# Optimization experiments

Hardware: AMD Instinct MI355X
Metric: run time of the kernel (lower is better)

The kernel has to match this reference:

```python
import jax, jax.numpy as jnp
import numpy as np

N_NODES = 50000


def gin_conv(x, src, dst, W, b, eps=0.0):
    # GINConv: nn((1+eps)*x_i + sum_{j in N(i)} x_j)
    agg = jax.ops.segment_sum(x[src], dst, num_segments=N_NODES)  # [N, D]
    h = (1.0 + eps) * x + agg
    return h @ W + b


def setup_inputs() -> dict:
    key = jax.random.key(0)
    ks = jax.random.split(key, 8)
    n, e = N_NODES, 800000
    d_in, d_h, d_out = 128, 128, 64
    feature = jax.random.normal(ks[0], (n, d_in), dtype=jnp.float32)
    edge_index = jax.random.randint(ks[1], (2, e), 0, n, dtype=jnp.int64)
    s1 = 1.0 / np.sqrt(d_in)
    sh = 1.0 / np.sqrt(d_h)
    W1 = jax.random.normal(ks[2], (d_in, d_h), dtype=jnp.float32) * s1
    b1 = jnp.zeros((d_h,), dtype=jnp.float32)
    Wh = jax.random.normal(ks[3], (d_h, d_h), dtype=jnp.float32) * sh
    bh = jnp.zeros((d_h,), dtype=jnp.float32)
    Wo = jax.random.normal(ks[4], (d_h, d_out), dtype=jnp.float32) * sh
    bo = jnp.zeros((d_out,), dtype=jnp.float32)
    return {"feature": feature, "edge_index": edge_index, "W1": W1, "b1": b1,
            "Wh": Wh, "bh": bh, "Wo": Wo, "bo": bo}


def reference(feature, edge_index, W1, b1, Wh, bh, Wo, bo):
    src, dst = edge_index[0], edge_index[1]
    x = gin_conv(feature, src, dst, W1, b1)
    x = jax.nn.relu(x)
    # one hidden layer (layer_num=3); dropout disabled (eval)
    x = gin_conv(x, src, dst, Wh, bh)
    x = jax.nn.relu(x)
    x = gin_conv(x, src, dst, Wo, bo)
    return jax.nn.log_softmax(x, axis=1)
```

## Files before the change

### kernel.cpp

```cpp
#include <hip/hip_runtime.h>

typedef short short8 __attribute__((ext_vector_type(8)));
typedef float f32x4 __attribute__((ext_vector_type(4)));


__device__ inline unsigned short f2bf(float f) {
    union { float f; unsigned u; } v; v.f = f;
    unsigned r = v.u + 0x7fffu + ((v.u >> 16) & 1u);
    return (unsigned short)(r >> 16);
}
__device__ inline unsigned pack2(float a, float b) {
    return (unsigned)f2bf(a) | ((unsigned)f2bf(b) << 16);
}
__device__ inline float bflo(unsigned u) { union { unsigned q; float f; } c; c.q = u << 16; return c.f; }
__device__ inline float bfhi(unsigned u) { union { unsigned q; float f; } c; c.q = u & 0xffff0000u; return c.f; }

#define ACC8(vv)                                     \
    acc[0] += bflo(vv.x); acc[1] += bfhi(vv.x);      \
    acc[2] += bflo(vv.y); acc[3] += bfhi(vv.y);      \
    acc[4] += bflo(vv.z); acc[5] += bfhi(vv.z);      \
    acc[6] += bflo(vv.w); acc[7] += bfhi(vv.w);

template <int TPN, typename F>
__device__ __forceinline__ void gather_acc(float acc[8], const uint4* __restrict__ x,
                                           int lane, int beg, int end, F geti) {
    int k = beg;
    for (; k + 8 <= end; k += 8) {
        int idx[8];
#pragma unroll
        for (int j = 0; j < 8; j++) idx[j] = geti(k + j);
        uint4 v[8];
#pragma unroll
        for (int j = 0; j < 8; j++) v[j] = x[(size_t)idx[j] * TPN + lane];
#pragma unroll
        for (int j = 0; j < 8; j++) { ACC8(v[j]) }
    }
    for (; k + 4 <= end; k += 4) {
        int i0 = geti(k), i1 = geti(k + 1), i2 = geti(k + 2), i3 = geti(k + 3);
        uint4 v0 = x[(size_t)i0 * TPN + lane];
        uint4 v1 = x[(size_t)i1 * TPN + lane];
        uint4 v2 = x[(size_t)i2 * TPN + lane];
        uint4 v3 = x[(size_t)i3 * TPN + lane];
        ACC8(v0) ACC8(v1) ACC8(v2) ACC8(v3)
    }
    for (; k < end; ++k) {
        uint4 v0 = x[(size_t)geti(k) * TPN + lane];
        ACC8(v0)
    }
}


#define EPB 2048
#define NE 8
#define BSH 9
#define MAXBKT 128
#define DCAP 10240

__global__ __launch_bounds__(256) void mega1(const int* __restrict__ dst, int* __restrict__ cnt2d,
                                             int e, int nbkt, int nblk,
                                             const float4* __restrict__ feat, uint2* __restrict__ featb,
                                             int cvtb, int nf4,
                                             const float* __restrict__ W1, const float* __restrict__ Wh,
                                             const float* __restrict__ Wo,
                                             unsigned short* __restrict__ W1t, unsigned short* __restrict__ Wht,
                                             unsigned short* __restrict__ Wot) {
    __shared__ int hist[MAXBKT];
    int t = threadIdx.x, b = blockIdx.x;
    if (b < nblk) {
        for (int j = t; j < nbkt; j += 256) hist[j] = 0;
        __syncthreads();
        int base = b * EPB;
#pragma unroll
        for (int j = 0; j < NE; j++) {
            int idx = base + t + 256 * j;
            if (idx < e) atomicAdd(&hist[dst[idx] >> BSH], 1);
        }
        __syncthreads();
        for (int j = t; j < nbkt; j += 256) cnt2d[j * nblk + b] = hist[j];
    } else if (b < nblk + cvtb) {
        int i = (b - nblk) * 256 + t;
        if (i < nf4) {
            float4 v = feat[i];
            featb[i] = make_uint2(pack2(v.x, v.y), pack2(v.z, v.w));
        }
    } else {
        int i = (b - nblk - cvtb) * 256 + t;
        if (i < 16384) {
            int k = i >> 7, nn = i & 127;
            W1t[nn * 128 + k] = f2bf(W1[i]);
        } else if (i < 32768) {
            int j = i - 16384, k = j >> 7, nn = j & 127;
            Wht[nn * 128 + k] = f2bf(Wh[j]);
        } else if (i < 40960) {
            int j = i - 32768, k = j >> 6, nn = j & 63;
            Wot[nn * 128 + k] = f2bf(Wo[j]);
        }
    }
}

__global__ __launch_bounds__(512) void scanB1(int* __restrict__ cnt2d, int* __restrict__ totals, int nblk) {
    __shared__ int s[512];
    int t = threadIdx.x, b = blockIdx.x;
    int v = (t < nblk) ? cnt2d[b * nblk + t] : 0;
    s[t] = v;
    __syncthreads();
    for (int off = 1; off < 512; off <<= 1) {
        int u = (t >= off) ? s[t - off] : 0;
        __syncthreads();
        s[t] += u;
        __syncthreads();
    }
    if (t < nblk) cnt2d[b * nblk + t] = s[t] - v;
    if (t == nblk - 1) totals[b] = s[t];
}

__global__ __launch_bounds__(128) void scanB2(const int* __restrict__ totals, int* __restrict__ bbase,
                                              int* __restrict__ row_ptr, int nbkt, int n, int e) {
    __shared__ int s[128];
    int t = threadIdx.x;
    int v = (t < nbkt) ? totals[t] : 0;
    s[t] = v;
    __syncthreads();
    for (int off = 1; off < 128; off <<= 1) {
        int u = (t >= off) ? s[t - off] : 0;
        __syncthreads();
        s[t] += u;
        __syncthreads();
    }
    if (t < nbkt) bbase[t] = s[t] - v;
    if (t == 0) row_ptr[n] = e;
}

__global__ __launch_bounds__(256) void binC(const int* __restrict__ src, const int* __restrict__ dst,
                                            const int* __restrict__ cnt2d, const int* __restrict__ bbase,
                                            unsigned* __restrict__ pairs, int e, int nbkt, int nblk) {
    __shared__ int hist[MAXBKT], loff[MAXBKT], cur[MAXBKT], gb[MAXBKT];
    __shared__ int sc[256];
    __shared__ unsigned sorted[EPB];
    int t = threadIdx.x, blk = blockIdx.x;
    for (int b = t; b < nbkt; b += 256) hist[b] = 0;
    __syncthreads();
    int base = blk * EPB;
    int cnt = min(EPB, e - base);
    unsigned packed[NE];
    int bb[NE];
#pragma unroll
    for (int j = 0; j < NE; j++) {
        int idx = base + t + 256 * j;
        bb[j] = -1;
        if (idx < e) {
            unsigned s0 = (unsigned)src[idx], d = (unsigned)dst[idx];
            int b = (int)(d >> BSH);
            bb[j] = b;
            packed[j] = s0 | ((d & ((1u << BSH) - 1)) << 16) | ((unsigned)b << 25);
            atomicAdd(&hist[b], 1);
        }
    }
    __syncthreads();
    int v = (t < nbkt) ? hist[t] : 0;
    sc[t] = v;
    __syncthreads();
    for (int off = 1; off < 256; off <<= 1) {
        int u = (t >= off) ? sc[t - off] : 0;
        __syncthreads();
        sc[t] += u;
        __syncthreads();
    }
    if (t < nbkt) {
        int ex = sc[t] - v;
        loff[t] = ex;
        cur[t] = ex;
        gb[t] = bbase[t] + cnt2d[t * nblk + blk];
    }
    __syncthreads();
#pragma unroll
    for (int j = 0; j < NE; j++) {
        if (bb[j] >= 0) {
            int r = atomicAdd(&cur[bb[j]], 1);
            sorted[r] = packed[j];
        }
    }
    __syncthreads();
    for (int i = t; i < cnt; i += 256) {
        unsigned w = sorted[i];
        int b = (int)(w >> 25);
        pairs[gb[b] + (i - loff[b])] = w;
    }
}

__global__ __launch_bounds__(512) void buildD(const unsigned* __restrict__ pairs,
                                              const int* __restrict__ totals, const int* __restrict__ bbase,
                                              int* __restrict__ row_ptr, unsigned short* __restrict__ csr, int n) {
    __shared__ int hist[512], off[512];
    __shared__ unsigned short lcsr[DCAP];
    int t = threadIdx.x, b = blockIdx.x;
    int cnt = totals[b], base = bbase[b];
    hist[t] = 0;
    __syncthreads();
    for (int i = t; i < cnt; i += 512)
        atomicAdd(&hist[(pairs[base + i] >> 16) & 511], 1);
    __syncthreads();
    int v = hist[t];
    off[t] = v;
    __syncthreads();
    for (int o = 1; o < 512; o <<= 1) {
        int u = (t >= o) ? off[t - o] : 0;
        __syncthreads();
        off[t] += u;
        __syncthreads();
    }
    int excl = off[t] - v;
    int node = (b << BSH) + t;
    if (node < n) row_ptr[node] = base + excl;
    __syncthreads();
    hist[t] = excl;
    __syncthreads();
    for (int i = t; i < cnt; i += 512) {
        unsigned w = pairs[base + i];
        int r = atomicAdd(&hist[(w >> 16) & 511], 1);
        if (r < DCAP) lcsr[r] = (unsigned short)(w & 0xFFFFu);
    }
    __syncthreads();
    int lim = min(cnt, DCAP);
    for (int i = t; i < lim; i += 512) csr[base + i] = lcsr[i];
}


#define ECAP 1024

template <bool SECOND>
__global__ __launch_bounds__(256) void fused_layer(
    const uint4* __restrict__ x, const int* __restrict__ row_ptr,
    const unsigned short* __restrict__ csr,
    const short8* __restrict__ Bt, const float* __restrict__ bias,
    unsigned short* __restrict__ out_h,
    const short8* __restrict__ Bt2,
    unsigned short* __restrict__ out_y,
    int n) {
    __shared__ unsigned short As[16][136];
    __shared__ unsigned short Hs[SECOND ? 16 : 1][SECOND ? 136 : 1];
    __shared__ unsigned short eidx[ECAP];

    int t = threadIdx.x;
    int nl = t >> 4, chunk = t & 15;
    int r0 = blockIdx.x * 16;
    int node = r0 + nl;

    int E0 = row_ptr[r0 < n ? r0 : n];
    int E1 = row_ptr[min(r0 + 16, n)];
    int ecnt = min(E1 - E0, ECAP);
    for (int i = t; i < ecnt; i += 256) eidx[i] = csr[E0 + i];
    __syncthreads();

    float acc[8] = {0.f, 0.f, 0.f, 0.f, 0.f, 0.f, 0.f, 0.f};
    if (node < n) {
        uint4 s0 = x[(size_t)node * 16 + chunk];
        ACC8(s0)
        int beg = row_ptr[node], end = row_ptr[node + 1];
        if (end - E0 <= ECAP) {
            gather_acc<16>(acc, x, chunk, beg - E0, end - E0,
                           [&](int k) { return (int)eidx[k]; });
        } else {
            gather_acc<16>(acc, x, chunk, beg, end,
                           [&](int k) { return (int)csr[k]; });
        }
    }
    uint4 packed;
    packed.x = pack2(acc[0], acc[1]); packed.y = pack2(acc[2], acc[3]);
    packed.z = pack2(acc[4], acc[5]); packed.w = pack2(acc[6], acc[7]);
    ((uint4*)&As[nl][0])[chunk] = packed;
    __syncthreads();

    int wid = t >> 6, lane = t & 63;
    int lm = lane & 15, lq = lane >> 4;

    short8 a[4];
#pragma unroll
    for (int kc = 0; kc < 4; kc++)
        a[kc] = *(const short8*)&As[lm][kc * 32 + lq * 8];

    f32x4 hacc[2];
#pragma unroll
    for (int nt = 0; nt < 2; nt++) hacc[nt] = (f32x4){0.f, 0.f, 0.f, 0.f};
#pragma unroll
    for (int nt = 0; nt < 2; nt++) {
        const short8* Br = Bt + (size_t)((wid * 2 + nt) * 16 + lm) * 16;
#pragma unroll
        for (int kc = 0; kc < 4; kc++)
            hacc[nt] = __builtin_amdgcn_mfma_f32_16x16x32_bf16(a[kc], Br[kc * 4 + lq], hacc[nt], 0, 0, 0);
    }

#pragma unroll
    for (int nt = 0; nt < 2; nt++) {
        int col = (wid * 2 + nt) * 16 + lm;
        float bv = bias[col];
#pragma unroll
        for (int i = 0; i < 4; i++) {
            int row = r0 + lq * 4 + i;
            float v = fmaxf(hacc[nt][i] + bv, 0.f);
            if (SECOND) {
                Hs[lq * 4 + i][col] = f2bf(v);
            } else if (row < n) {
                out_h[(size_t)row * 128 + col] = f2bf(v);
            }
        }
    }

    if (SECOND) {
        __syncthreads();
        short8 a2[4];
#pragma unroll
        for (int kc = 0; kc < 4; kc++)
            a2[kc] = *(const short8*)&Hs[lm][kc * 32 + lq * 8];
        f32x4 yacc = (f32x4){0.f, 0.f, 0.f, 0.f};
        const short8* Br2 = Bt2 + (size_t)(wid * 16 + lm) * 16;
#pragma unroll
        for (int kc = 0; kc < 4; kc++)
            yacc = __builtin_amdgcn_mfma_f32_16x16x32_bf16(a2[kc], Br2[kc * 4 + lq], yacc, 0, 0, 0);
        int col = wid * 16 + lm;
#pragma unroll
        for (int i = 0; i < 4; i++) {
            int row = r0 + lq * 4 + i;
            if (row < n) out_y[(size_t)row * 64 + col] = f2bf(yacc[i]);
        }
    }
}


#define ECAP2 1536

__global__ __launch_bounds__(256) void agg_lsm(
    const uint4* __restrict__ x, float* __restrict__ out,
    const int* __restrict__ row_ptr, const unsigned short* __restrict__ csr,
    const float* __restrict__ bo, int n) {
    __shared__ unsigned short eidx[ECAP2];
    int t = threadIdx.x;
    int r0 = blockIdx.x * 32;
    int node = r0 + (t >> 3), lane = t & 7;

    int E0 = row_ptr[r0 < n ? r0 : n];
    int E1 = row_ptr[min(r0 + 32, n)];
    int ecnt = min(E1 - E0, ECAP2);
    for (int i = t; i < ecnt; i += 256) eidx[i] = csr[E0 + i];
    __syncthreads();

    if (node >= n) return;
    uint4 s0 = x[(size_t)node * 8 + lane];
    float acc[8] = { bflo(s0.x), bfhi(s0.x), bflo(s0.y), bfhi(s0.y),
                     bflo(s0.z), bfhi(s0.z), bflo(s0.w), bfhi(s0.w) };
    int beg = row_ptr[node], end = row_ptr[node + 1];
    if (end - E0 <= ECAP2) {
        gather_acc<8>(acc, x, lane, beg - E0, end - E0,
                      [&](int k) { return (int)eidx[k]; });
    } else {
        gather_acc<8>(acc, x, lane, beg, end,
                      [&](int k) { return (int)csr[k]; });
    }

    const float4* bo4 = (const float4*)bo;
    float4 bA = bo4[lane * 2], bB = bo4[lane * 2 + 1];
    acc[0] += bA.x; acc[1] += bA.y; acc[2] += bA.z; acc[3] += bA.w;
    acc[4] += bB.x; acc[5] += bB.y; acc[6] += bB.z; acc[7] += bB.w;
    float m = acc[0];
#pragma unroll
    for (int j = 1; j < 8; j++) m = fmaxf(m, acc[j]);
#pragma unroll
    for (int off = 1; off < 8; off <<= 1) m = fmaxf(m, __shfl_xor(m, off, 64));
    float s = 0.f;
#pragma unroll
    for (int j = 0; j < 8; j++) s += __expf(acc[j] - m);
#pragma unroll
    for (int off = 1; off < 8; off <<= 1) s += __shfl_xor(s, off, 64);
    float ls = m + __logf(s);
    float4 o0 = make_float4(acc[0] - ls, acc[1] - ls, acc[2] - ls, acc[3] - ls);
    float4 o1 = make_float4(acc[4] - ls, acc[5] - ls, acc[6] - ls, acc[7] - ls);
    float4* op = (float4*)(out + (size_t)node * 64 + lane * 8);
    op[0] = o0;
    op[1] = o1;
}


extern "C" void kernel_launch(void* const* d_in, const int* in_sizes, int n_in,
                              void* d_out, int out_size, void* d_ws, size_t ws_size,
                              hipStream_t stream) {
    const float* feature = (const float*)d_in[0];
    const int*   edges   = (const int*)d_in[1];
    const float* W1 = (const float*)d_in[2];
    const float* b1 = (const float*)d_in[3];
    const float* Wh = (const float*)d_in[4];
    const float* bh = (const float*)d_in[5];
    const float* Wo = (const float*)d_in[6];
    const float* bo = (const float*)d_in[7];

    int n = in_sizes[0] / 128;
    int e = in_sizes[1] / 2;
    const int* src = edges;
    const int* dst = edges + e;

    int nbkt = (n + 511) >> BSH;
    int nblk = (e + EPB - 1) / EPB;
    int nf4 = n * 32;
    int cvtb = (nf4 + 255) / 256;

    char* ws = (char*)d_ws;
    auto take = [&](size_t bytes) {
        char* p = ws;
        ws += (bytes + 255) & ~(size_t)255;
        return p;
    };
    int* cnt2d   = (int*)take((size_t)nbkt * nblk * 4);
    int* totals  = (int*)take((size_t)nbkt * 4);
    int* bbase   = (int*)take((size_t)(nbkt + 1) * 4);
    int* row_ptr = (int*)take((size_t)(n + 1) * 4);
    unsigned* pairs = (unsigned*)take((size_t)e * 4);
    unsigned short* csr = (unsigned short*)take((size_t)e * 2);
    unsigned short* featb = (unsigned short*)take((size_t)n * 128 * 2);
    unsigned short* hb    = (unsigned short*)take((size_t)n * 128 * 2);
    unsigned short* yb    = (unsigned short*)take((size_t)n * 64 * 2);
    unsigned short* W1t = (unsigned short*)take(128 * 128 * 2);
    unsigned short* Wht = (unsigned short*)take(128 * 128 * 2);
    unsigned short* Wot = (unsigned short*)take(64 * 128 * 2);

    mega1<<<nblk + cvtb + 160, 256, 0, stream>>>(
        dst, cnt2d, e, nbkt, nblk,
        (const float4*)feature, (uint2*)featb, cvtb, nf4,
        W1, Wh, Wo, W1t, Wht, Wot);
    scanB1<<<nbkt, 512, 0, stream>>>(cnt2d, totals, nblk);
    scanB2<<<1, 128, 0, stream>>>(totals, bbase, row_ptr, nbkt, n, e);
    binC<<<nblk, 256, 0, stream>>>(src, dst, cnt2d, bbase, pairs, e, nbkt, nblk);
    buildD<<<nbkt, 512, 0, stream>>>(pairs, totals, bbase, row_ptr, csr, n);

    int fblocks = (n + 15) / 16;

    fused_layer<false><<<fblocks, 256, 0, stream>>>(
        (const uint4*)featb, row_ptr, csr, (const short8*)W1t, b1,
        hb, nullptr, nullptr, n);

    fused_layer<true><<<fblocks, 256, 0, stream>>>(
        (const uint4*)hb, row_ptr, csr, (const short8*)Wht, bh,
        nullptr, (const short8*)Wot, yb, n);

    agg_lsm<<<(n + 31) / 32, 256, 0, stream>>>(
        (const uint4*)yb, (float*)d_out, row_ptr, csr, bo, n);
}
```

Before: 208.9 us.

## Split fused aggregate+GEMM into column-quarter aggregation and separate MFMA GEMM kernels

Replaces the fused gather+matmul layer kernels with a separate aggregation kernel and a standalone MFMA GEMM. The aggregation kernel splits the feature columns into 64-byte quarters per block, so each block gathers only part of each row, which is meant to improve cache locality and parallelism. The GEMM then reads the aggregated bf16 rows back from global memory. The final layer writes fp32 aggregates for a separate log-softmax kernel. This adds extra global round-trips and kernel launches in exchange for a narrower, more cache-friendly gather.

```diff
diff --git a/kernel.cpp b/kernel.cpp
--- a/kernel.cpp
+++ b/kernel.cpp
@@ -2,6 +2,7 @@
 
 typedef short short8 __attribute__((ext_vector_type(8)));
 typedef float f32x4 __attribute__((ext_vector_type(4)));
+typedef unsigned u32x4 __attribute__((ext_vector_type(4)));
 
 
 __device__ inline unsigned short f2bf(float f) {
@@ -226,141 +227,140 @@
 }
 
 
-#define ECAP 1024
-
-template <bool SECOND>
-__global__ __launch_bounds__(256) void fused_layer(
-    const uint4* __restrict__ x, const int* __restrict__ row_ptr,
-    const unsigned short* __restrict__ csr,
-    const short8* __restrict__ Bt, const float* __restrict__ bias,
-    unsigned short* __restrict__ out_h,
-    const short8* __restrict__ Bt2,
-    unsigned short* __restrict__ out_y,
-    int n) {
-    __shared__ unsigned short As[16][136];
-    __shared__ unsigned short Hs[SECOND ? 16 : 1][SECOND ? 136 : 1];
-    __shared__ unsigned short eidx[ECAP];
-
+#define QECAP 2048
+
+template <int TPN, bool OUTF32>
+__global__ __launch_bounds__(256) void agg_split(
+    const uint4* __restrict__ x, void* __restrict__ outp,
+    const int* __restrict__ row_ptr, const unsigned short* __restrict__ csr,
+    int n, int qblocks) {
+    constexpr int NQ = TPN / 4;
+    __shared__ unsigned short eidx[QECAP];
+    int q = (int)(blockIdx.x % NQ);
+    int nb = (int)(blockIdx.x / NQ);
     int t = threadIdx.x;
-    int nl = t >> 4, chunk = t & 15;
-    int r0 = blockIdx.x * 16;
-    int node = r0 + nl;
-
-    int E0 = row_ptr[r0 < n ? r0 : n];
-    int E1 = row_ptr[min(r0 + 16, n)];
-    int ecnt = min(E1 - E0, ECAP);
-    for (int i = t; i < ecnt; i += 256) eidx[i] = csr[E0 + i];
-    __syncthreads();
+    int r0 = nb * 64;
+
+    int E0 = row_ptr[min(r0, n)], E1 = row_ptr[min(r0 + 64, n)];
+    int ecnt = min(E1 - E0, QECAP);
+    for (int i = t; i < ecnt; i += 256)
+        eidx[i] = __builtin_nontemporal_load(&csr[E0 + i]);
+    __syncthreads();
+
+    int lane = t & 3, slot = t >> 2;
+    int node = r0 + slot;
+    if (node >= n) return;
+    int chunk = q * 4 + lane;
 
     float acc[8] = {0.f, 0.f, 0.f, 0.f, 0.f, 0.f, 0.f, 0.f};
-    if (node < n) {
-        uint4 s0 = x[(size_t)node * 16 + chunk];
-        ACC8(s0)
-        int beg = row_ptr[node], end = row_ptr[node + 1];
-        if (end - E0 <= ECAP) {
-            gather_acc<16>(acc, x, chunk, beg - E0, end - E0,
-                           [&](int k) { return (int)eidx[k]; });
-        } else {
-            gather_acc<16>(acc, x, chunk, beg, end,
-                           [&](int k) { return (int)csr[k]; });
-        }
-    }
-    uint4 packed;
-    packed.x = pack2(acc[0], acc[1]); packed.y = pack2(acc[2], acc[3]);
-    packed.z = pack2(acc[4], acc[5]); packed.w = pack2(acc[6], acc[7]);
-    ((uint4*)&As[nl][0])[chunk] = packed;
-    __syncthreads();
-
-    int wid = t >> 6, lane = t & 63;
-    int lm = lane & 15, lq = lane >> 4;
-
+    uint4 s0 = x[(size_t)node * TPN + chunk];
+    ACC8(s0)
+    int beg = row_ptr[node], end = row_ptr[node + 1];
+    if (E1 - E0 <= QECAP) {
+        gather_acc<TPN>(acc, x, chunk, beg - E0, end - E0,
+                        [&](int k) { return (int)eidx[k]; });
+    } else {
+        gather_acc<TPN>(acc, x, chunk, beg, end,
+                        [&](int k) { return (int)csr[k]; });
+    }
+
+    if (OUTF32) {
+        f32x4* o = (f32x4*)outp + (size_t)node * (TPN * 2) + chunk * 2;
+        f32x4 o0 = {acc[0], acc[1], acc[2], acc[3]};
+        f32x4 o1 = {acc[4], acc[5], acc[6], acc[7]};
+        __builtin_nontemporal_store(o0, o);
+        __builtin_nontemporal_store(o1, o + 1);
+    } else {
+        u32x4 pk = {pack2(acc[0], acc[1]), pack2(acc[2], acc[3]),
+                    pack2(acc[4], acc[5]), pack2(acc[6], acc[7])};
+        __builtin_nontemporal_store(pk, (u32x4*)outp + (size_t)node * TPN + chunk);
+    }
+}
+
+
+template <int OUT, bool SECOND>
+__global__ __launch_bounds__(256) void gemm_mfma(
+    const short8* __restrict__ A, const short8* __restrict__ Bt,
+    const float* __restrict__ bias, unsigned short* __restrict__ outp,
+    const short8* __restrict__ Bt2, unsigned short* __restrict__ out_y, int n) {
+    constexpr int NT = OUT / 16;
+    __shared__ unsigned short Hs[SECOND ? 4 : 1][16][136];
+    int t = threadIdx.x;
+    int wid = t >> 6, lane = t & 63, lm = lane & 15, lq = lane >> 4;
+    int r0 = blockIdx.x * 64 + wid * 16;
+    int arow = min(r0 + lm, n - 1);
+    const short8* Ar = A + (size_t)arow * 16;
     short8 a[4];
 #pragma unroll
-    for (int kc = 0; kc < 4; kc++)
-        a[kc] = *(const short8*)&As[lm][kc * 32 + lq * 8];
-
-    f32x4 hacc[2];
-#pragma unroll
-    for (int nt = 0; nt < 2; nt++) hacc[nt] = (f32x4){0.f, 0.f, 0.f, 0.f};
-#pragma unroll
-    for (int nt = 0; nt < 2; nt++) {
-        const short8* Br = Bt + (size_t)((wid * 2 + nt) * 16 + lm) * 16;
+    for (int kc = 0; kc < 4; kc++) a[kc] = __builtin_nontemporal_load(&Ar[kc * 4 + lq]);
+
+    f32x4 acc[NT];
+#pragma unroll
+    for (int nt = 0; nt < NT; nt++) acc[nt] = (f32x4){0.f, 0.f, 0.f, 0.f};
+#pragma unroll
+    for (int nt = 0; nt < NT; nt++) {
+        const short8* Br = Bt + (size_t)(nt * 16 + lm) * 16;
 #pragma unroll
         for (int kc = 0; kc < 4; kc++)
-            hacc[nt] = __builtin_amdgcn_mfma_f32_16x16x32_bf16(a[kc], Br[kc * 4 + lq], hacc[nt], 0, 0, 0);
-    }
-
-#pragma unroll
-    for (int nt = 0; nt < 2; nt++) {
-        int col = (wid * 2 + nt) * 16 + lm;
+            acc[nt] = __builtin_amdgcn_mfma_f32_16x16x32_bf16(a[kc], Br[kc * 4 + lq], acc[nt], 0, 0, 0);
+    }
+
+#pragma unroll
+    for (int nt = 0; nt < NT; nt++) {
+        int col = nt * 16 + lm;
         float bv = bias[col];
 #pragma unroll
         for (int i = 0; i < 4; i++) {
             int row = r0 + lq * 4 + i;
-            float v = fmaxf(hacc[nt][i] + bv, 0.f);
+            float v = fmaxf(acc[nt][i] + bv, 0.f);
             if (SECOND) {
-                Hs[lq * 4 + i][col] = f2bf(v);
+                Hs[wid][lq * 4 + i][col] = f2bf(v);
             } else if (row < n) {
-                out_h[(size_t)row * 128 + col] = f2bf(v);
+                outp[(size_t)row * OUT + col] = f2bf(v);
             }
         }
     }
 
     if (SECOND) {
-        __syncthreads();
         short8 a2[4];
 #pragma unroll
         for (int kc = 0; kc < 4; kc++)
-            a2[kc] = *(const short8*)&Hs[lm][kc * 32 + lq * 8];
-        f32x4 yacc = (f32x4){0.f, 0.f, 0.f, 0.f};
-        const short8* Br2 = Bt2 + (size_t)(wid * 16 + lm) * 16;
-#pragma unroll
-        for (int kc = 0; kc < 4; kc++)
-            yacc = __builtin_amdgcn_mfma_f32_16x16x32_bf16(a2[kc], Br2[kc * 4 + lq], yacc, 0, 0, 0);
-        int col = wid * 16 + lm;
-#pragma unroll
-        for (int i = 0; i < 4; i++) {
-            int row = r0 + lq * 4 + i;
-            if (row < n) out_y[(size_t)row * 64 + col] = f2bf(yacc[i]);
-        }
-    }
-}
-
-
-#define ECAP2 1536
-
-__global__ __launch_bounds__(256) void agg_lsm(
-    const uint4* __restrict__ x, float* __restrict__ out,
-    const int* __restrict__ row_ptr, const unsigned short* __restrict__ csr,
-    const float* __restrict__ bo, int n) {
-    __shared__ unsigned short eidx[ECAP2];
+            a2[kc] = *(const short8*)&Hs[wid][lm][kc * 32 + lq * 8];
+        f32x4 yacc[4];
+#pragma unroll
+        for (int ct = 0; ct < 4; ct++) yacc[ct] = (f32x4){0.f, 0.f, 0.f, 0.f};
+#pragma unroll
+        for (int ct = 0; ct < 4; ct++) {
+            const short8* Br2 = Bt2 + (size_t)(ct * 16 + lm) * 16;
+#pragma unroll
+            for (int kc = 0; kc < 4; kc++)
+                yacc[ct] = __builtin_amdgcn_mfma_f32_16x16x32_bf16(a2[kc], Br2[kc * 4 + lq], yacc[ct], 0, 0, 0);
+        }
+#pragma unroll
+        for (int ct = 0; ct < 4; ct++) {
+            int col = ct * 16 + lm;
+#pragma unroll
+            for (int i = 0; i < 4; i++) {
+                int row = r0 + lq * 4 + i;
+                if (row < n) out_y[(size_t)row * 64 + col] = f2bf(yacc[ct][i]);
+            }
+        }
+    }
+}
+
+
+__global__ __launch_bounds__(256) void lsm_kernel(const float4* __restrict__ z,
+                                                  const float* __restrict__ bo,
+                                                  float* __restrict__ out, int n) {
     int t = threadIdx.x;
-    int r0 = blockIdx.x * 32;
-    int node = r0 + (t >> 3), lane = t & 7;
-
-    int E0 = row_ptr[r0 < n ? r0 : n];
-    int E1 = row_ptr[min(r0 + 32, n)];
-    int ecnt = min(E1 - E0, ECAP2);
-    for (int i = t; i < ecnt; i += 256) eidx[i] = csr[E0 + i];
-    __syncthreads();
-
+    int node = blockIdx.x * 32 + (t >> 3), lane = t & 7;
     if (node >= n) return;
-    uint4 s0 = x[(size_t)node * 8 + lane];
-    float acc[8] = { bflo(s0.x), bfhi(s0.x), bflo(s0.y), bfhi(s0.y),
-                     bflo(s0.z), bfhi(s0.z), bflo(s0.w), bfhi(s0.w) };
-    int beg = row_ptr[node], end = row_ptr[node + 1];
-    if (end - E0 <= ECAP2) {
-        gather_acc<8>(acc, x, lane, beg - E0, end - E0,
-                      [&](int k) { return (int)eidx[k]; });
-    } else {
-        gather_acc<8>(acc, x, lane, beg, end,
-                      [&](int k) { return (int)csr[k]; });
-    }
-
+    float4 v0 = z[(size_t)node * 16 + lane * 2];
+    float4 v1 = z[(size_t)node * 16 + lane * 2 + 1];
     const float4* bo4 = (const float4*)bo;
     float4 bA = bo4[lane * 2], bB = bo4[lane * 2 + 1];
-    acc[0] += bA.x; acc[1] += bA.y; acc[2] += bA.z; acc[3] += bA.w;
-    acc[4] += bB.x; acc[5] += bB.y; acc[6] += bB.z; acc[7] += bB.w;
+    float acc[8] = { v0.x + bA.x, v0.y + bA.y, v0.z + bA.z, v0.w + bA.w,
+                     v1.x + bB.x, v1.y + bB.y, v1.z + bB.z, v1.w + bB.w };
     float m = acc[0];
 #pragma unroll
     for (int j = 1; j < 8; j++) m = fmaxf(m, acc[j]);
@@ -372,11 +372,9 @@
 #pragma unroll
     for (int off = 1; off < 8; off <<= 1) s += __shfl_xor(s, off, 64);
     float ls = m + __logf(s);
-    float4 o0 = make_float4(acc[0] - ls, acc[1] - ls, acc[2] - ls, acc[3] - ls);
-    float4 o1 = make_float4(acc[4] - ls, acc[5] - ls, acc[6] - ls, acc[7] - ls);
     float4* op = (float4*)(out + (size_t)node * 64 + lane * 8);
-    op[0] = o0;
-    op[1] = o1;
+    op[0] = make_float4(acc[0] - ls, acc[1] - ls, acc[2] - ls, acc[3] - ls);
+    op[1] = make_float4(acc[4] - ls, acc[5] - ls, acc[6] - ls, acc[7] - ls);
 }
 
 
@@ -415,8 +413,10 @@
     unsigned* pairs = (unsigned*)take((size_t)e * 4);
     unsigned short* csr = (unsigned short*)take((size_t)e * 2);
     unsigned short* featb = (unsigned short*)take((size_t)n * 128 * 2);
+    unsigned short* aggb  = (unsigned short*)take((size_t)n * 128 * 2);
     unsigned short* hb    = (unsigned short*)take((size_t)n * 128 * 2);
     unsigned short* yb    = (unsigned short*)take((size_t)n * 64 * 2);
+    float*          zf    = (float*)take((size_t)n * 64 * 4);
     unsigned short* W1t = (unsigned short*)take(128 * 128 * 2);
     unsigned short* Wht = (unsigned short*)take(128 * 128 * 2);
     unsigned short* Wot = (unsigned short*)take(64 * 128 * 2);
@@ -430,16 +430,20 @@
     binC<<<nblk, 256, 0, stream>>>(src, dst, cnt2d, bbase, pairs, e, nbkt, nblk);
     buildD<<<nbkt, 512, 0, stream>>>(pairs, totals, bbase, row_ptr, csr, n);
 
-    int fblocks = (n + 15) / 16;
-
-    fused_layer<false><<<fblocks, 256, 0, stream>>>(
-        (const uint4*)featb, row_ptr, csr, (const short8*)W1t, b1,
-        hb, nullptr, nullptr, n);
-
-    fused_layer<true><<<fblocks, 256, 0, stream>>>(
-        (const uint4*)hb, row_ptr, csr, (const short8*)Wht, bh,
-        nullptr, (const short8*)Wot, yb, n);
-
-    agg_lsm<<<(n + 31) / 32, 256, 0, stream>>>(
-        (const uint4*)yb, (float*)d_out, row_ptr, csr, bo, n);
-}
+    int qblocks = (n + 63) / 64;
+
+    agg_split<16, false><<<qblocks * 4, 256, 0, stream>>>(
+        (const uint4*)featb, aggb, row_ptr, csr, n, qblocks);
+    gemm_mfma<128, false><<<qblocks, 256, 0, stream>>>(
+        (const short8*)aggb, (const short8*)W1t, b1, hb, nullptr, nullptr, n);
+
+    agg_split<16, false><<<qblocks * 4, 256, 0, stream>>>(
+        (const uint4*)hb, aggb, row_ptr, csr, n, qblocks);
+    gemm_mfma<128, true><<<qblocks, 256, 0, stream>>>(
+        (const short8*)aggb, (const short8*)Wht, bh, nullptr, (const short8*)Wot, yb, n);
+
+    agg_split<8, true><<<qblocks * 2, 256, 0, stream>>>(
+        (const uint4*)yb, zf, row_ptr, csr, n, qblocks);
+    lsm_kernel<<<(n + 31) / 32, 256, 0, stream>>>(
+        (const float4*)zf, bo, (float*)d_out, n);
+}
```

New measurement: 263.1 us. +25.9%, slower.

## Replace two-pass bucket scan with fixed-capacity buckets and global atomic cursors

Applied to the files above, without the earlier changes.

The histogram, two scan kernels and the binning kernel are merged into one pass. Each edge block claims space in fixed-capacity per-bucket regions through global atomic cursors, which removes three kernel launches and the second read of the edge list. Because buckets are no longer contiguous, a row_end array replaces row_ptr[n+1], and the consumers use it. This assumes no bucket exceeds BCAP edges, which holds for uniform random graphs but is a capacity risk for skewed ones. Edge order within a bucket also becomes nondeterministic.

```diff
diff --git a/kernel.cpp b/kernel.cpp
--- a/kernel.cpp
+++ b/kernel.cpp
@@ -55,36 +55,77 @@
 #define BSH 9
 #define MAXBKT 128
 #define DCAP 10240
-
-__global__ __launch_bounds__(256) void mega1(const int* __restrict__ dst, int* __restrict__ cnt2d,
-                                             int e, int nbkt, int nblk,
-                                             const float4* __restrict__ feat, uint2* __restrict__ featb,
-                                             int cvtb, int nf4,
-                                             const float* __restrict__ W1, const float* __restrict__ Wh,
-                                             const float* __restrict__ Wo,
-                                             unsigned short* __restrict__ W1t, unsigned short* __restrict__ Wht,
-                                             unsigned short* __restrict__ Wot) {
-    __shared__ int hist[MAXBKT];
-    int t = threadIdx.x, b = blockIdx.x;
-    if (b < nblk) {
-        for (int j = t; j < nbkt; j += 256) hist[j] = 0;
-        __syncthreads();
-        int base = b * EPB;
+#define BCAP 16384
+
+__global__ __launch_bounds__(256) void megaA(
+    const int* __restrict__ src, const int* __restrict__ dst,
+    int* __restrict__ cursor, unsigned* __restrict__ pairs,
+    int e, int nbkt, int nblk,
+    const float4* __restrict__ feat, uint2* __restrict__ featb, int cvtb, int nf4,
+    const float* __restrict__ W1, const float* __restrict__ Wh, const float* __restrict__ Wo,
+    unsigned short* __restrict__ W1t, unsigned short* __restrict__ Wht,
+    unsigned short* __restrict__ Wot) {
+    __shared__ int hist[MAXBKT], loff[MAXBKT], cur[MAXBKT], gb[MAXBKT];
+    __shared__ int sc[256];
+    __shared__ unsigned sorted[EPB];
+    int t = threadIdx.x, blk = blockIdx.x;
+    if (blk < nblk) {
+        for (int b = t; b < nbkt; b += 256) hist[b] = 0;
+        __syncthreads();
+        int base = blk * EPB;
+        int cnt = min(EPB, e - base);
+        unsigned packed[NE];
+        int bb[NE];
 #pragma unroll
         for (int j = 0; j < NE; j++) {
             int idx = base + t + 256 * j;
-            if (idx < e) atomicAdd(&hist[dst[idx] >> BSH], 1);
-        }
-        __syncthreads();
-        for (int j = t; j < nbkt; j += 256) cnt2d[j * nblk + b] = hist[j];
-    } else if (b < nblk + cvtb) {
-        int i = (b - nblk) * 256 + t;
+            bb[j] = -1;
+            if (idx < e) {
+                unsigned s0 = (unsigned)src[idx], d = (unsigned)dst[idx];
+                int b = (int)(d >> BSH);
+                bb[j] = b;
+                packed[j] = s0 | ((d & ((1u << BSH) - 1)) << 16) | ((unsigned)b << 25);
+                atomicAdd(&hist[b], 1);
+            }
+        }
+        __syncthreads();
+        int v = (t < nbkt) ? hist[t] : 0;
+        sc[t] = v;
+        __syncthreads();
+        for (int off = 1; off < 256; off <<= 1) {
+            int u = (t >= off) ? sc[t - off] : 0;
+            __syncthreads();
+            sc[t] += u;
+            __syncthreads();
+        }
+        if (t < nbkt) {
+            int ex = sc[t] - v;
+            loff[t] = ex;
+            cur[t] = ex;
+            gb[t] = t * BCAP + (v ? atomicAdd(&cursor[t], v) : atomicAdd(&cursor[t], 0));
+        }
+        __syncthreads();
+#pragma unroll
+        for (int j = 0; j < NE; j++) {
+            if (bb[j] >= 0) {
+                int r = atomicAdd(&cur[bb[j]], 1);
+                sorted[r] = packed[j];
+            }
+        }
+        __syncthreads();
+        for (int i = t; i < cnt; i += 256) {
+            unsigned w = sorted[i];
+            int b = (int)(w >> 25);
+            pairs[gb[b] + (i - loff[b])] = w;
+        }
+    } else if (blk < nblk + cvtb) {
+        int i = (blk - nblk) * 256 + t;
         if (i < nf4) {
             float4 v = feat[i];
             featb[i] = make_uint2(pack2(v.x, v.y), pack2(v.z, v.w));
         }
     } else {
-        int i = (b - nblk - cvtb) * 256 + t;
+        int i = (blk - nblk - cvtb) * 256 + t;
         if (i < 16384) {
             int k = i >> 7, nn = i & 127;
             W1t[nn * 128 + k] = f2bf(W1[i]);
@@ -98,103 +139,14 @@
     }
 }
 
-__global__ __launch_bounds__(512) void scanB1(int* __restrict__ cnt2d, int* __restrict__ totals, int nblk) {
-    __shared__ int s[512];
-    int t = threadIdx.x, b = blockIdx.x;
-    int v = (t < nblk) ? cnt2d[b * nblk + t] : 0;
-    s[t] = v;
-    __syncthreads();
-    for (int off = 1; off < 512; off <<= 1) {
-        int u = (t >= off) ? s[t - off] : 0;
-        __syncthreads();
-        s[t] += u;
-        __syncthreads();
-    }
-    if (t < nblk) cnt2d[b * nblk + t] = s[t] - v;
-    if (t == nblk - 1) totals[b] = s[t];
-}
-
-__global__ __launch_bounds__(128) void scanB2(const int* __restrict__ totals, int* __restrict__ bbase,
-                                              int* __restrict__ row_ptr, int nbkt, int n, int e) {
-    __shared__ int s[128];
-    int t = threadIdx.x;
-    int v = (t < nbkt) ? totals[t] : 0;
-    s[t] = v;
-    __syncthreads();
-    for (int off = 1; off < 128; off <<= 1) {
-        int u = (t >= off) ? s[t - off] : 0;
-        __syncthreads();
-        s[t] += u;
-        __syncthreads();
-    }
-    if (t < nbkt) bbase[t] = s[t] - v;
-    if (t == 0) row_ptr[n] = e;
-}
-
-__global__ __launch_bounds__(256) void binC(const int* __restrict__ src, const int* __restrict__ dst,
-                                            const int* __restrict__ cnt2d, const int* __restrict__ bbase,
-                                            unsigned* __restrict__ pairs, int e, int nbkt, int nblk) {
-    __shared__ int hist[MAXBKT], loff[MAXBKT], cur[MAXBKT], gb[MAXBKT];
-    __shared__ int sc[256];
-    __shared__ unsigned sorted[EPB];
-    int t = threadIdx.x, blk = blockIdx.x;
-    for (int b = t; b < nbkt; b += 256) hist[b] = 0;
-    __syncthreads();
-    int base = blk * EPB;
-    int cnt = min(EPB, e - base);
-    unsigned packed[NE];
-    int bb[NE];
-#pragma unroll
-    for (int j = 0; j < NE; j++) {
-        int idx = base + t + 256 * j;
-        bb[j] = -1;
-        if (idx < e) {
-            unsigned s0 = (unsigned)src[idx], d = (unsigned)dst[idx];
-            int b = (int)(d >> BSH);
-            bb[j] = b;
-            packed[j] = s0 | ((d & ((1u << BSH) - 1)) << 16) | ((unsigned)b << 25);
-            atomicAdd(&hist[b], 1);
-        }
-    }
-    __syncthreads();
-    int v = (t < nbkt) ? hist[t] : 0;
-    sc[t] = v;
-    __syncthreads();
-    for (int off = 1; off < 256; off <<= 1) {
-        int u = (t >= off) ? sc[t - off] : 0;
-        __syncthreads();
-        sc[t] += u;
-        __syncthreads();
-    }
-    if (t < nbkt) {
-        int ex = sc[t] - v;
-        loff[t] = ex;
-        cur[t] = ex;
-        gb[t] = bbase[t] + cnt2d[t * nblk + blk];
-    }
-    __syncthreads();
-#pragma unroll
-    for (int j = 0; j < NE; j++) {
-        if (bb[j] >= 0) {
-            int r = atomicAdd(&cur[bb[j]], 1);
-            sorted[r] = packed[j];
-        }
-    }
-    __syncthreads();
-    for (int i = t; i < cnt; i += 256) {
-        unsigned w = sorted[i];
-        int b = (int)(w >> 25);
-        pairs[gb[b] + (i - loff[b])] = w;
-    }
-}
-
 __global__ __launch_bounds__(512) void buildD(const unsigned* __restrict__ pairs,
-                                              const int* __restrict__ totals, const int* __restrict__ bbase,
-                                              int* __restrict__ row_ptr, unsigned short* __restrict__ csr, int n) {
+                                              const int* __restrict__ cursor,
+                                              int* __restrict__ row_ptr, int* __restrict__ row_end,
+                                              unsigned short* __restrict__ csr, int n) {
     __shared__ int hist[512], off[512];
     __shared__ unsigned short lcsr[DCAP];
     int t = threadIdx.x, b = blockIdx.x;
-    int cnt = totals[b], base = bbase[b];
+    int cnt = cursor[b], base = b * BCAP;
     hist[t] = 0;
     __syncthreads();
     for (int i = t; i < cnt; i += 512)
@@ -211,7 +163,10 @@
     }
     int excl = off[t] - v;
     int node = (b << BSH) + t;
-    if (node < n) row_ptr[node] = base + excl;
+    if (node < n) {
+        row_ptr[node] = base + excl;
+        row_end[node] = base + off[t];
+    }
     __syncthreads();
     hist[t] = excl;
     __syncthreads();
@@ -231,7 +186,7 @@
 template <bool SECOND>
 __global__ __launch_bounds__(256) void fused_layer(
     const uint4* __restrict__ x, const int* __restrict__ row_ptr,
-    const unsigned short* __restrict__ csr,
+    const int* __restrict__ row_end, const unsigned short* __restrict__ csr,
     const short8* __restrict__ Bt, const float* __restrict__ bias,
     unsigned short* __restrict__ out_h,
     const short8* __restrict__ Bt2,
@@ -246,8 +201,8 @@
     int r0 = blockIdx.x * 16;
     int node = r0 + nl;
 
-    int E0 = row_ptr[r0 < n ? r0 : n];
-    int E1 = row_ptr[min(r0 + 16, n)];
+    int E0 = row_ptr[min(r0, n - 1)];
+    int E1 = row_end[min(r0 + 15, n - 1)];
     int ecnt = min(E1 - E0, ECAP);
     for (int i = t; i < ecnt; i += 256) eidx[i] = csr[E0 + i];
     __syncthreads();
@@ -256,8 +211,8 @@
     if (node < n) {
         uint4 s0 = x[(size_t)node * 16 + chunk];
         ACC8(s0)
-        int beg = row_ptr[node], end = row_ptr[node + 1];
-        if (end - E0 <= ECAP) {
+        int beg = row_ptr[node], end = row_end[node];
+        if (E1 - E0 <= ECAP) {
             gather_acc<16>(acc, x, chunk, beg - E0, end - E0,
                            [&](int k) { return (int)eidx[k]; });
         } else {
@@ -331,15 +286,15 @@
 
 __global__ __launch_bounds__(256) void agg_lsm(
     const uint4* __restrict__ x, float* __restrict__ out,
-    const int* __restrict__ row_ptr, const unsigned short* __restrict__ csr,
-    const float* __restrict__ bo, int n) {
+    const int* __restrict__ row_ptr, const int* __restrict__ row_end,
+    const unsigned short* __restrict__ csr, const float* __restrict__ bo, int n) {
     __shared__ unsigned short eidx[ECAP2];
     int t = threadIdx.x;
     int r0 = blockIdx.x * 32;
     int node = r0 + (t >> 3), lane = t & 7;
 
-    int E0 = row_ptr[r0 < n ? r0 : n];
-    int E1 = row_ptr[min(r0 + 32, n)];
+    int E0 = row_ptr[min(r0, n - 1)];
+    int E1 = row_end[min(r0 + 31, n - 1)];
     int ecnt = min(E1 - E0, ECAP2);
     for (int i = t; i < ecnt; i += 256) eidx[i] = csr[E0 + i];
     __syncthreads();
@@ -348,8 +303,8 @@
     uint4 s0 = x[(size_t)node * 8 + lane];
     float acc[8] = { bflo(s0.x), bfhi(s0.x), bflo(s0.y), bfhi(s0.y),
                      bflo(s0.z), bfhi(s0.z), bflo(s0.w), bfhi(s0.w) };
-    int beg = row_ptr[node], end = row_ptr[node + 1];
-    if (end - E0 <= ECAP2) {
+    int beg = row_ptr[node], end = row_end[node];
+    if (E1 - E0 <= ECAP2) {
         gather_acc<8>(acc, x, lane, beg - E0, end - E0,
                       [&](int k) { return (int)eidx[k]; });
     } else {
@@ -408,12 +363,11 @@
         ws += (bytes + 255) & ~(size_t)255;
         return p;
     };
-    int* cnt2d   = (int*)take((size_t)nbkt * nblk * 4);
-    int* totals  = (int*)take((size_t)nbkt * 4);
-    int* bbase   = (int*)take((size_t)(nbkt + 1) * 4);
-    int* row_ptr = (int*)take((size_t)(n + 1) * 4);
-    unsigned* pairs = (unsigned*)take((size_t)e * 4);
-    unsigned short* csr = (unsigned short*)take((size_t)e * 2);
+    int* cursor  = (int*)take((size_t)nbkt * 4);
+    int* row_ptr = (int*)take((size_t)n * 4);
+    int* row_end = (int*)take((size_t)n * 4);
+    unsigned* pairs = (unsigned*)take((size_t)nbkt * BCAP * 4);
+    unsigned short* csr = (unsigned short*)take((size_t)nbkt * BCAP * 2);
     unsigned short* featb = (unsigned short*)take((size_t)n * 128 * 2);
     unsigned short* hb    = (unsigned short*)take((size_t)n * 128 * 2);
     unsigned short* yb    = (unsigned short*)take((size_t)n * 64 * 2);
@@ -421,25 +375,23 @@
     unsigned short* Wht = (unsigned short*)take(128 * 128 * 2);
     unsigned short* Wot = (unsigned short*)take(64 * 128 * 2);
 
-    mega1<<<nblk + cvtb + 160, 256, 0, stream>>>(
-        dst, cnt2d, e, nbkt, nblk,
+    hipMemsetAsync(cursor, 0, (size_t)nbkt * 4, stream);
+    megaA<<<nblk + cvtb + 160, 256, 0, stream>>>(
+        src, dst, cursor, pairs, e, nbkt, nblk,
         (const float4*)feature, (uint2*)featb, cvtb, nf4,
         W1, Wh, Wo, W1t, Wht, Wot);
-    scanB1<<<nbkt, 512, 0, stream>>>(cnt2d, totals, nblk);
-    scanB2<<<1, 128, 0, stream>>>(totals, bbase, row_ptr, nbkt, n, e);
-    binC<<<nblk, 256, 0, stream>>>(src, dst, cnt2d, bbase, pairs, e, nbkt, nblk);
-    buildD<<<nbkt, 512, 0, stream>>>(pairs, totals, bbase, row_ptr, csr, n);
+    buildD<<<nbkt, 512, 0, stream>>>(pairs, cursor, row_ptr, row_end, csr, n);
 
     int fblocks = (n + 15) / 16;
 
     fused_layer<false><<<fblocks, 256, 0, stream>>>(
-        (const uint4*)featb, row_ptr, csr, (const short8*)W1t, b1,
+        (const uint4*)featb, row_ptr, row_end, csr, (const short8*)W1t, b1,
         hb, nullptr, nullptr, n);
 
     fused_layer<true><<<fblocks, 256, 0, stream>>>(
-        (const uint4*)hb, row_ptr, csr, (const short8*)Wht, bh,
+        (const uint4*)hb, row_ptr, row_end, csr, (const short8*)Wht, bh,
         nullptr, (const short8*)Wot, yb, n);
 
     agg_lsm<<<(n + 31) / 32, 256, 0, stream>>>(
-        (const uint4*)yb, (float*)d_out, row_ptr, csr, bo, n);
-}
+        (const uint4*)yb, (float*)d_out, row_ptr, row_end, csr, bo, n);
+}
```

Result: no change. 209.6 us (+0.3%).
